# Kernel tuning notes

Measured on AMD Instinct MI355X. Metric: run time of the kernel, lower is better.

Reference implementation:

```python
import jax, jax.numpy as jnp
import numpy as np

N_CLI, N_AGG, E, D, L = 100000, 1000, 1600000, 128, 3


def setup_inputs() -> dict:
    key = jax.random.key(0)
    ks = jax.random.split(key, 16)
    inp = {
        'x_clients': jax.random.normal(ks[0], (N_CLI, D), jnp.float32),
        'x_agg': jax.random.normal(ks[1], (N_AGG, D), jnp.float32),
        'c2a_src': jax.random.randint(ks[2], (E,), 0, N_CLI, jnp.int32),
        'c2a_dst': jax.random.randint(ks[3], (E,), 0, N_AGG, jnp.int32),
        'a2c_src': jax.random.randint(ks[4], (E,), 0, N_AGG, jnp.int32),
        'a2c_dst': jax.random.randint(ks[5], (E,), 0, N_CLI, jnp.int32),
    }
    s = 1.0 / np.sqrt(D)
    # stacked per-layer SAGE params for each edge type: W_l (on aggregated msg), W_r (on dst), b
    inp['Wl_c2a'] = jax.random.uniform(ks[6], (L, D, D), jnp.float32, -s, s)
    inp['Wr_c2a'] = jax.random.uniform(ks[7], (L, D, D), jnp.float32, -s, s)
    inp['b_c2a'] = jax.random.uniform(ks[8], (L, D), jnp.float32, -s, s)
    inp['Wl_a2c'] = jax.random.uniform(ks[9], (L, D, D), jnp.float32, -s, s)
    inp['Wr_a2c'] = jax.random.uniform(ks[10], (L, D, D), jnp.float32, -s, s)
    inp['b_a2c'] = jax.random.uniform(ks[11], (L, D), jnp.float32, -s, s)
    inp['W_lin'] = jax.random.uniform(ks[12], (D, 1), jnp.float32, -s, s)
    inp['b_lin'] = jax.random.uniform(ks[13], (1,), jnp.float32, -s, s)
    return inp


def _sage(x_src, x_dst, src, dst, Wl, Wr, b, n_dst):
    # mean aggregation of gathered source features onto dst nodes
    msg = x_src[src]                                        # [E, D]
    summed = jax.ops.segment_sum(msg, dst, num_segments=n_dst)
    cnt = jax.ops.segment_sum(jnp.ones((src.shape[0], 1), x_src.dtype), dst, num_segments=n_dst)
    mean = summed / jnp.maximum(cnt, 1.0)
    return mean @ Wl + x_dst @ Wr + b


def _leaky(x):
    return jnp.where(x >= 0, x, 0.1 * x)


def reference(x_clients, x_agg, c2a_src, c2a_dst, a2c_src, a2c_dst,
              Wl_c2a, Wr_c2a, b_c2a, Wl_a2c, Wr_a2c, b_a2c, W_lin, b_lin):
    xc, xa = x_clients, x_agg
    for l in range(L):
        new_a = _sage(xc, xa, c2a_src, c2a_dst, Wl_c2a[l], Wr_c2a[l], b_c2a[l], N_AGG)
        new_c = _sage(xa, xc, a2c_src, a2c_dst, Wl_a2c[l], Wr_a2c[l], b_a2c[l], N_CLI)
        xa, xc = _leaky(new_a), _leaky(new_c)
    return (xc @ W_lin + b_lin).squeeze(1)
```

## Files before the change

### kernel.cpp

```cpp
#include <hip/hip_runtime.h>

#define D      128
#define NCLI   100000
#define NAGG   1000
#define NLAYER 3
#define NBKT   98
#define NC2A   63
#define NRNG   8
#define NBIN   (NAGG * NRNG)
#define RMAGIC 343598u
#define NHIST  512
#define NCVTX  (NCLI * D / 4 / 256)
#define NCVTW  ((NLAYER * D * D + 255) / 256)
#define NROWT  (NCLI / 32)
#define CPB    391

typedef short bf16x8 __attribute__((ext_vector_type(8)));
typedef float f32x16 __attribute__((ext_vector_type(16)));

static __device__ __forceinline__ float leaky(float x) { return x >= 0.f ? x : 0.1f * x; }

static __device__ __forceinline__ unsigned bf16_rn(float f) {
    unsigned u = __float_as_uint(f);
    return (u + 0x7fffu + ((u >> 16) & 1u)) >> 16;
}
static __device__ __forceinline__ float bf_val(unsigned h) { return __uint_as_float(h << 16); }
static __device__ __forceinline__ unsigned pack_bf2(float lo, float hi) {
    return bf16_rn(lo) | (bf16_rn(hi) << 16);
}
static __device__ __forceinline__ float bf_lo(unsigned v) { return __uint_as_float(v << 16); }
static __device__ __forceinline__ float bf_hi(unsigned v) { return __uint_as_float(v & 0xffff0000u); }

__global__ __launch_bounds__(256) void prep(const int* __restrict__ c2a_src,
                                            const int* __restrict__ c2a_dst,
                                            const int* __restrict__ a2c_dst, int E,
                                            int* __restrict__ cnt_ar, int* __restrict__ bcnt,
                                            const float4* __restrict__ X4,
                                            uint2* __restrict__ xhi, uint2* __restrict__ xlo,
                                            const float* __restrict__ W,
                                            unsigned short* __restrict__ Wt) {
    __shared__ int h[NBIN + NBKT];
    int bid = blockIdx.x;
    if (bid < NHIST) {
        for (int i = threadIdx.x; i < NBIN + NBKT; i += 256) h[i] = 0;
        __syncthreads();
        int stride = NHIST * 256;
        for (int e = bid * 256 + threadIdx.x; e < E; e += stride) {
            int s = c2a_src[e];
            int bin = c2a_dst[e] * NRNG + (int)__umulhi((unsigned)s, RMAGIC);
            atomicAdd(&h[bin], 1);
            atomicAdd(&h[NBIN + (a2c_dst[e] >> 10)], 1);
        }
        __syncthreads();
        for (int i = threadIdx.x; i < NBIN; i += 256)
            if (h[i]) atomicAdd(&cnt_ar[i], h[i]);
        for (int i = threadIdx.x; i < NBKT; i += 256)
            if (h[NBIN + i]) atomicAdd(&bcnt[i], h[NBIN + i]);
    } else if (bid < NHIST + NCVTX) {
        int t = (bid - NHIST) * 256 + threadIdx.x;
        float4 f = X4[t];
        unsigned h0 = bf16_rn(f.x), h1 = bf16_rn(f.y), h2 = bf16_rn(f.z), h3 = bf16_rn(f.w);
        xhi[t] = make_uint2(h0 | (h1 << 16), h2 | (h3 << 16));
        xlo[t] = make_uint2(pack_bf2(f.x - bf_val(h0), f.y - bf_val(h1)),
                            pack_bf2(f.z - bf_val(h2), f.w - bf_val(h3)));
    } else {
        int idx = (bid - NHIST - NCVTX) * 256 + threadIdx.x;
        if (idx >= NLAYER * D * D) return;
        int layer = idx >> 14, rem = idx & (D * D - 1);
        int k = rem >> 7, n = rem & 127;
        float w = W[layer * D * D + k * D + n];
        unsigned hh = bf16_rn(w);
        unsigned short* base = Wt + layer * 2 * D * D;
        base[n * D + k] = (unsigned short)hh;
        base[D * D + n * D + k] = (unsigned short)bf16_rn(w - bf_val(hh));
    }
}

__global__ void scan_both(const int* __restrict__ cnt_ar, int* __restrict__ rp_ar,
                          const int* __restrict__ bcnt,
                          int* __restrict__ brp, int* __restrict__ bcur,
                          int* __restrict__ ccur) {
    __shared__ int sh[1024];
    int t = threadIdx.x;
    if (blockIdx.x == 0) {
        int v[8];
        int s = 0;
#pragma unroll
        for (int j = 0; j < 8; j++) {
            int idx = t * 8 + j;
            v[j] = (idx < NBIN) ? cnt_ar[idx] : 0;
            s += v[j];
        }
        sh[t] = s;
        __syncthreads();
        for (int off = 1; off < 1024; off <<= 1) {
            int x = (t >= off) ? sh[t - off] : 0;
            __syncthreads();
            sh[t] += x;
            __syncthreads();
        }
        int run = sh[t] - s;
#pragma unroll
        for (int j = 0; j < 8; j++) {
            int idx = t * 8 + j;
            if (idx < NBIN) rp_ar[idx] = run;
            run += v[j];
        }
        if (t == 1023) rp_ar[NBIN] = sh[1023];
        __syncthreads();
        if (t < NC2A) ccur[t] = rp_ar[t * 128];
    } else {
        int v = (t < NBKT) ? bcnt[t] : 0;
        sh[t] = v;
        __syncthreads();
        for (int off = 1; off < 1024; off <<= 1) {
            int x = (t >= off) ? sh[t - off] : 0;
            __syncthreads();
            sh[t] += x;
            __syncthreads();
        }
        if (t == 0) { brp[0] = 0; bcur[0] = 0; }
        if (t < NBKT) {
            brp[t + 1] = sh[t];
            if (t + 1 < NBKT) bcur[t + 1] = sh[t];
        }
    }
}

__global__ __launch_bounds__(1024) void scatter_coarse(const int* __restrict__ c2a_src,
                                                       const int* __restrict__ c2a_dst,
                                                       const int* __restrict__ a2c_src,
                                                       const int* __restrict__ a2c_dst, int E,
                                                       int* __restrict__ ccur,
                                                       int* __restrict__ tmp1,
                                                       int* __restrict__ bcur,
                                                       int* __restrict__ tmp2) {
    __shared__ int h[NBKT], base[NBKT];
    int tid = threadIdx.x;
    if (blockIdx.x < 256) {
        int chunk = (E + 255) / 256;
        int e0 = blockIdx.x * chunk;
        int e1 = min(E, e0 + chunk);
        for (int i = tid; i < NC2A; i += 1024) h[i] = 0;
        __syncthreads();
        for (int e = e0 + tid; e < e1; e += 1024) {
            int s = c2a_src[e];
            int bin = c2a_dst[e] * NRNG + (int)__umulhi((unsigned)s, RMAGIC);
            atomicAdd(&h[bin >> 7], 1);
        }
        __syncthreads();
        for (int i = tid; i < NC2A; i += 1024) {
            int c = h[i];
            base[i] = c ? atomicAdd(&ccur[i], c) : 0;
        }
        __syncthreads();
        for (int e = e0 + tid; e < e1; e += 1024) {
            int s = c2a_src[e];
            int bin = c2a_dst[e] * NRNG + (int)__umulhi((unsigned)s, RMAGIC);
            int pos = atomicAdd(&base[bin >> 7], 1);
            tmp1[pos] = (bin << 17) | s;
        }
    } else {
        int bid = blockIdx.x - 256;
        int chunk = (E + 255) / 256;
        int e0 = bid * chunk;
        int e1 = min(E, e0 + chunk);
        for (int i = tid; i < NBKT; i += 1024) h[i] = 0;
        __syncthreads();
        for (int e = e0 + tid; e < e1; e += 1024) atomicAdd(&h[a2c_dst[e] >> 10], 1);
        __syncthreads();
        for (int i = tid; i < NBKT; i += 1024) {
            int c = h[i];
            base[i] = c ? atomicAdd(&bcur[i], c) : 0;
        }
        __syncthreads();
        for (int e = e0 + tid; e < e1; e += 1024) {
            int d = a2c_dst[e];
            int pos = atomicAdd(&base[d >> 10], 1);
            tmp2[pos] = ((d & 1023) << 10) | a2c_src[e];
        }
    }
}

__global__ __launch_bounds__(1024) void refine(const int* __restrict__ rp_ar,
                                               const int* __restrict__ tmp1,
                                               int* __restrict__ col_c2a,
                                               const int* __restrict__ brp,
                                               const int* __restrict__ tmp2,
                                               int* __restrict__ rp_c,
                                               int* __restrict__ col_a2c) {
    int tid = threadIdx.x;
    if (blockIdx.x < NC2A) {
        __shared__ int lcur[128];
        int c = blockIdx.x;
        int b0 = c * 128;
        int nb = min(128, NBIN - b0);
        if (tid < nb) lcur[tid] = rp_ar[b0 + tid];
        int beg = rp_ar[b0];
        int end = rp_ar[min(b0 + 128, NBIN)];
        __syncthreads();
        for (int e = beg + tid; e < end; e += 1024) {
            int v = tmp1[e];
            int pos = atomicAdd(&lcur[(v >> 17) - b0], 1);
            col_c2a[pos] = v & 0x1FFFF;
        }
    } else {
        __shared__ int h2[1024], cur2[1024];
        int b = blockIdx.x - NC2A;
        int beg = brp[b], end = brp[b + 1];
        h2[tid] = 0;
        __syncthreads();
        for (int e = beg + tid; e < end; e += 1024) atomicAdd(&h2[tmp2[e] >> 10], 1);
        __syncthreads();
        cur2[tid] = h2[tid];
        __syncthreads();
        for (int off = 1; off < 1024; off <<= 1) {
            int x = (tid >= off) ? cur2[tid - off] : 0;
            __syncthreads();
            cur2[tid] += x;
            __syncthreads();
        }
        int start = beg + cur2[tid] - h2[tid];
        int c = b * 1024 + tid;
        if (c < NCLI) rp_c[c] = start;
        cur2[tid] = start;
        if (b == NBKT - 1 && tid == 0) rp_c[NCLI] = end;
        __syncthreads();
        for (int e = beg + tid; e < end; e += 1024) {
            int p = tmp2[e];
            int pos = atomicAdd(&cur2[p >> 10], 1);
            col_a2c[pos] = p & 1023;
        }
    }
}


__global__ __launch_bounds__(512) void gather_mean(const unsigned* __restrict__ tbl,
                                                   const int* __restrict__ rp_ar,
                                                   const int* __restrict__ col,
                                                   float* __restrict__ psum) {
    __shared__ float part[4][8][D];
    int quad = blockIdx.x >> 3, r = blockIdx.x & 7;
    int tid = threadIdx.x;
    int a = tid >> 7;
    int sub = (tid >> 4) & 7;
    int sl = tid & 15;
    const uint4* tbl4 = (const uint4*)tbl;
    int agg = quad * 4 + a;
    int bin = agg * NRNG + r;
    int beg = rp_ar[bin], end = rp_ar[bin + 1];
    float f0 = 0, f1 = 0, f2 = 0, f3 = 0, f4 = 0, f5 = 0, f6 = 0, f7 = 0;
    int e = beg + sub;
    for (; e + 8 < end; e += 16) {
        int s0 = col[e];
        int s1 = col[e + 8];
        uint4 v0 = tbl4[(s0 << 4) + sl];
        uint4 v1 = tbl4[(s1 << 4) + sl];
        f0 += bf_lo(v0.x); f1 += bf_hi(v0.x); f2 += bf_lo(v0.y); f3 += bf_hi(v0.y);
        f4 += bf_lo(v0.z); f5 += bf_hi(v0.z); f6 += bf_lo(v0.w); f7 += bf_hi(v0.w);
        f0 += bf_lo(v1.x); f1 += bf_hi(v1.x); f2 += bf_lo(v1.y); f3 += bf_hi(v1.y);
        f4 += bf_lo(v1.z); f5 += bf_hi(v1.z); f6 += bf_lo(v1.w); f7 += bf_hi(v1.w);
    }
    if (e < end) {
        int s0 = col[e];
        uint4 v0 = tbl4[(s0 << 4) + sl];
        f0 += bf_lo(v0.x); f1 += bf_hi(v0.x); f2 += bf_lo(v0.y); f3 += bf_hi(v0.y);
        f4 += bf_lo(v0.z); f5 += bf_hi(v0.z); f6 += bf_lo(v0.w); f7 += bf_hi(v0.w);
    }
    float* pr = &part[a][sub][sl * 8];
    pr[0] = f0; pr[1] = f1; pr[2] = f2; pr[3] = f3;
    pr[4] = f4; pr[5] = f5; pr[6] = f6; pr[7] = f7;
    __syncthreads();
    int c = tid & 127;
    float s = 0.f;
#pragma unroll
    for (int g = 0; g < 8; g++) s += part[a][g][c];
    psum[((size_t)agg * NRNG + r) * D + c] = s;
}

template <int LAST>
__global__ __launch_bounds__(128) void combine_agg(const float* __restrict__ psum,
                                                   const int* __restrict__ rp_ar,
                                                   const float* xa_old,
                                                   const float* __restrict__ Wl_a2c,
                                                   const float* __restrict__ Wl_c2a,
                                                   const float* __restrict__ Wr_c2a,
                                                   const float* __restrict__ b_c2a,
                                                   unsigned short* __restrict__ ya_bf,
                                                   float* xa_out) {
    __shared__ float mr[D], xr[D];
    int i = blockIdx.x, j = threadIdx.x;
    if (LAST) {
        xr[j] = xa_old[i * D + j];
        __syncthreads();
        float accy = 0.f;
#pragma unroll 4
        for (int k = 0; k < D; k++) accy += xr[k] * Wl_a2c[k * D + j];
        ya_bf[i * D + j] = (unsigned short)bf16_rn(accy);
        return;
    }
    const float* pr = psum + (size_t)i * NRNG * D + j;
    float s = 0.f;
#pragma unroll
    for (int r = 0; r < NRNG; r++) s += pr[r * D];
    int deg = rp_ar[i * NRNG + NRNG] - rp_ar[i * NRNG];
    mr[j] = s / fmaxf((float)deg, 1.f);
    xr[j] = xa_old[i * D + j];
    __syncthreads();
    float accy = 0.f, accn = b_c2a[j];
#pragma unroll 4
    for (int k = 0; k < D; k++) {
        accy += xr[k] * Wl_a2c[k * D + j];
        accn += mr[k] * Wl_c2a[k * D + j] + xr[k] * Wr_c2a[k * D + j];
    }
    ya_bf[i * D + j] = (unsigned short)bf16_rn(accy);
    xa_out[i * D + j] = leaky(accn);
}

__global__ __launch_bounds__(256) void gemm_y(const unsigned short* __restrict__ Ahi,
                                              const unsigned short* __restrict__ Alo,
                                              const unsigned short* __restrict__ Wt,
                                              const float* __restrict__ bias,
                                              float* __restrict__ Yb) {
    int tid = threadIdx.x;
    int wave = tid >> 6, lane = tid & 63;
    int cl = lane & 31, kh = lane >> 5;
    int n0 = wave * 32;
    int m0 = blockIdx.x * 32;
    float bv = bias[n0 + cl];
    f32x16 acc;
#pragma unroll
    for (int qq = 0; qq < 16; qq++) acc[qq] = bv;
    {
        const unsigned short* Wlo_ = Wt + D * D;
        const unsigned short* ar = Ahi + (size_t)(m0 + cl) * D + kh * 8;
        const unsigned short* al = Alo + (size_t)(m0 + cl) * D + kh * 8;
        const unsigned short* wh = Wt + (size_t)(n0 + cl) * D + kh * 8;
        const unsigned short* wl = Wlo_ + (size_t)(n0 + cl) * D + kh * 8;
#pragma unroll
        for (int kc = 0; kc < 8; kc++) {
            bf16x8 ahi = *(const bf16x8*)(ar + kc * 16);
            bf16x8 alo = *(const bf16x8*)(al + kc * 16);
            bf16x8 bh = *(const bf16x8*)(wh + kc * 16);
            bf16x8 bl = *(const bf16x8*)(wl + kc * 16);
            acc = __builtin_amdgcn_mfma_f32_32x32x16_bf16(ahi, bh, acc, 0, 0, 0);
            acc = __builtin_amdgcn_mfma_f32_32x32x16_bf16(alo, bh, acc, 0, 0, 0);
            acc = __builtin_amdgcn_mfma_f32_32x32x16_bf16(ahi, bl, acc, 0, 0, 0);
        }
    }
    float* yb = Yb + (size_t)m0 * D + n0 + cl;
#pragma unroll
    for (int reg = 0; reg < 16; reg++) {
        int row = (reg & 3) + 8 * (reg >> 2) + 4 * kh;
        yb[(size_t)row * D] = acc[reg];
    }
}

template <int LAST>
__global__ __launch_bounds__(1024) void agg_big(const unsigned short* __restrict__ ya,
                                                const int* __restrict__ rowptr,
                                                const int* __restrict__ col,
                                                const float* __restrict__ Yb,
                                                unsigned* __restrict__ xhi,
                                                unsigned* __restrict__ xlo,
                                                const float* __restrict__ Wlin,
                                                const float* __restrict__ blin,
                                                float* __restrict__ out) {
    __shared__ uint4 yast4[NAGG * 9];
    int tid = threadIdx.x;
    int wave = tid >> 6, lane = tid & 63;
    int g = lane >> 3, q = lane & 7;
    int m0 = blockIdx.x * CPB;
    const uint4* ya4g = (const uint4*)ya;
    float dacc[4] = {0.f, 0.f, 0.f, 0.f};
#pragma unroll
    for (int h = 0; h < 2; h++) {
        if (h) __syncthreads();
        for (int i = tid; i < NAGG * 8; i += 1024) {
            int row = i >> 3, qq = i & 7;
            yast4[row * 9 + qq] = ya4g[(row << 4) + (h << 3) + qq];
        }
        __syncthreads();
#pragma unroll
        for (int cc = 0; cc < 4; cc++) {
            int c_local = (wave * 8 + g) * 4 + cc;
            int gid = m0 + c_local;
            bool act = (c_local < CPB) && (gid < NCLI);
            int beg = 0, end = 0;
            if (act) { beg = rowptr[gid]; end = rowptr[gid + 1]; }
            float s0 = 0, s1 = 0, s2 = 0, s3 = 0, s4 = 0, s5 = 0, s6 = 0, s7 = 0;
            for (int ch = beg; ch < end; ch += 8) {
                int ec = col[min(ch + q, end - 1)];
                int lim = min(8, end - ch);
#pragma unroll
                for (int j = 0; j < 8; j++) {
                    if (j < lim) {
                        int r = __shfl(ec, j, 8);
                        uint4 v = yast4[r * 9 + q];
                        s0 += bf_lo(v.x); s1 += bf_hi(v.x);
                        s2 += bf_lo(v.y); s3 += bf_hi(v.y);
                        s4 += bf_lo(v.z); s5 += bf_hi(v.z);
                        s6 += bf_lo(v.w); s7 += bf_hi(v.w);
                    }
                }
            }
            if (act) {
                float inv = 1.f / fmaxf((float)(end - beg), 1.f);
                const float4* yb4 =
                    (const float4*)(Yb + (size_t)gid * D + h * 64 + q * 8);
                float4 y0 = yb4[0], y1 = yb4[1];
                float r0 = leaky(y0.x + s0 * inv);
                float r1 = leaky(y0.y + s1 * inv);
                float r2 = leaky(y0.z + s2 * inv);
                float r3 = leaky(y0.w + s3 * inv);
                float r4 = leaky(y1.x + s4 * inv);
                float r5 = leaky(y1.y + s5 * inv);
                float r6 = leaky(y1.z + s6 * inv);
                float r7 = leaky(y1.w + s7 * inv);
                if (LAST) {
                    float4 w0 = *(const float4*)&Wlin[h * 64 + q * 8];
                    float4 w1 = *(const float4*)&Wlin[h * 64 + q * 8 + 4];
                    dacc[cc] += r0 * w0.x + r1 * w0.y + r2 * w0.z + r3 * w0.w +
                                r4 * w1.x + r5 * w1.y + r6 * w1.z + r7 * w1.w;
                    if (h == 1) {
                        float v = dacc[cc];
#pragma unroll
                        for (int off = 4; off > 0; off >>= 1) v += __shfl_down(v, off, 8);
                        if (q == 0) out[gid] = v + blin[0];
                    }
                } else {
                    unsigned h0 = bf16_rn(r0), h1 = bf16_rn(r1);
                    unsigned h2 = bf16_rn(r2), h3 = bf16_rn(r3);
                    unsigned h4 = bf16_rn(r4), h5 = bf16_rn(r5);
                    unsigned h6 = bf16_rn(r6), h7 = bf16_rn(r7);
                    uint4 hi, lo;
                    hi.x = h0 | (h1 << 16); hi.y = h2 | (h3 << 16);
                    hi.z = h4 | (h5 << 16); hi.w = h6 | (h7 << 16);
                    lo.x = pack_bf2(r0 - bf_val(h0), r1 - bf_val(h1));
                    lo.y = pack_bf2(r2 - bf_val(h2), r3 - bf_val(h3));
                    lo.z = pack_bf2(r4 - bf_val(h4), r5 - bf_val(h5));
                    lo.w = pack_bf2(r6 - bf_val(h6), r7 - bf_val(h7));
                    ((uint4*)xhi)[(gid << 4) + (h << 3) + q] = hi;
                    ((uint4*)xlo)[(gid << 4) + (h << 3) + q] = lo;
                }
            }
        }
    }
}

extern "C" void kernel_launch(void* const* d_in, const int* in_sizes, int n_in,
                              void* d_out, int out_size, void* d_ws, size_t ws_size,
                              hipStream_t stream) {
    const float* x_clients = (const float*)d_in[0];
    const float* x_agg     = (const float*)d_in[1];
    const int*   c2a_src   = (const int*)d_in[2];
    const int*   c2a_dst   = (const int*)d_in[3];
    const int*   a2c_src   = (const int*)d_in[4];
    const int*   a2c_dst   = (const int*)d_in[5];
    const float* Wl_c2a    = (const float*)d_in[6];
    const float* Wr_c2a    = (const float*)d_in[7];
    const float* b_c2a     = (const float*)d_in[8];
    const float* Wl_a2c    = (const float*)d_in[9];
    const float* Wr_a2c    = (const float*)d_in[10];
    const float* b_a2c     = (const float*)d_in[11];
    const float* W_lin     = (const float*)d_in[12];
    const float* b_lin     = (const float*)d_in[13];
    float* out = (float*)d_out;
    const int E = in_sizes[2];

    char* p = (char*)d_ws;
    auto alloc = [&](size_t bytes) {
        char* r = p;
        p += (bytes + 255) & ~(size_t)255;
        return r;
    };
    float*    Yb    = (float*)alloc(sizeof(float) * NCLI * D);
    unsigned* xc_hi = (unsigned*)alloc(sizeof(unsigned) * NCLI * 64);
    unsigned* xc_lo = (unsigned*)alloc(sizeof(unsigned) * NCLI * 64);
    float*    xa    = (float*)alloc(sizeof(float) * NAGG * D);
    unsigned short* ya_bf = (unsigned short*)alloc(sizeof(unsigned short) * NAGG * D);
    unsigned short* Wt = (unsigned short*)alloc(sizeof(unsigned short) * NLAYER * 2 * D * D);
    float* psum  = (float*)alloc(sizeof(float) * NAGG * NRNG * D);
    int* cnt_ar = (int*)alloc(sizeof(int) * (NBIN + NBKT));
    int* bcnt  = cnt_ar + NBIN;
    int* rp_ar = (int*)alloc(sizeof(int) * (NBIN + 1));
    int* brp   = (int*)alloc(sizeof(int) * (NBKT + 1));
    int* bcur  = (int*)alloc(sizeof(int) * NBKT);
    int* ccur  = (int*)alloc(sizeof(int) * NC2A);
    int* rp_c  = (int*)alloc(sizeof(int) * (NCLI + 1));
    int* col_c2a = (int*)alloc(sizeof(int) * E);
    int* col_a2c = (int*)alloc(sizeof(int) * E);
    int* tmp1 = (int*)Yb;
    int* tmp2 = tmp1 + E;

    hipMemsetAsync(cnt_ar, 0, sizeof(int) * (NBIN + NBKT), stream);

    prep<<<NHIST + NCVTX + NCVTW, 256, 0, stream>>>(c2a_src, c2a_dst, a2c_dst, E, cnt_ar, bcnt,
                                                    (const float4*)x_clients,
                                                    (uint2*)xc_hi, (uint2*)xc_lo,
                                                    Wr_a2c, Wt);
    scan_both<<<2, 1024, 0, stream>>>(cnt_ar, rp_ar, bcnt, brp, bcur, ccur);
    scatter_coarse<<<512, 1024, 0, stream>>>(c2a_src, c2a_dst, a2c_src, a2c_dst, E,
                                             ccur, tmp1, bcur, tmp2);
    refine<<<NC2A + NBKT, 1024, 0, stream>>>(rp_ar, tmp1, col_c2a, brp, tmp2, rp_c, col_a2c);

    const float* xa_old = x_agg;
    for (int l = 0; l < NLAYER; l++) {
        if (l < NLAYER - 1) {
            gather_mean<<<(NAGG / 4) * NRNG, 512, 0, stream>>>(xc_hi, rp_ar, col_c2a, psum);
            combine_agg<0><<<NAGG, 128, 0, stream>>>(psum, rp_ar, xa_old,
                                                     Wl_a2c + l * D * D, Wl_c2a + l * D * D,
                                                     Wr_c2a + l * D * D, b_c2a + l * D,
                                                     ya_bf, xa);
            gemm_y<<<NROWT, 256, 0, stream>>>(
                (const unsigned short*)xc_hi, (const unsigned short*)xc_lo,
                Wt + l * 2 * D * D, b_a2c + l * D, Yb);
            agg_big<0><<<256, 1024, 0, stream>>>(ya_bf, rp_c, col_a2c, Yb,
                                                 xc_hi, xc_lo, nullptr, nullptr, nullptr);
        } else {
            combine_agg<1><<<NAGG, 128, 0, stream>>>(psum, rp_ar, xa_old,
                                                     Wl_a2c + l * D * D, Wl_c2a + l * D * D,
                                                     Wr_c2a + l * D * D, b_c2a + l * D,
                                                     ya_bf, xa);
            gemm_y<<<NROWT, 256, 0, stream>>>(
                (const unsigned short*)xc_hi, (const unsigned short*)xc_lo,
                Wt + l * 2 * D * D, b_a2c + l * D, Yb);
            agg_big<1><<<256, 1024, 0, stream>>>(ya_bf, rp_c, col_a2c, Yb,
                                                 nullptr, nullptr, W_lin, b_lin, out);
        }
        xa_old = xa;
    }
}
```

Baseline: 609.5 us.

## Fuse gather_mean and gemm_y into one heterogeneous per-layer launch

Merges the independent c2a gather-mean and the client GEMM (Yb = xc@Wr + b) into a single kernel whose blocks are partitioned by blockIdx: GEMM tiles (two 32-row tiles per 512-thread block), gather blocks, and in the last layer small blocks computing ya = xa@Wl_a2c. This lets the memory-bound gather overlap with the MFMA-bound GEMM and removes launches and serialization between them. In exchange, register and LDS footprint are set by the largest branch, which may lower occupancy for the GEMM part. Early-return of odd tail tiles happens before no barrier in the GEMM branch, so it stays safe.

```diff
diff --git a/kernel.cpp b/kernel.cpp
--- a/kernel.cpp
+++ b/kernel.cpp
@@ -13,6 +13,9 @@
 #define NCVTX  (NCLI * D / 4 / 256)
 #define NCVTW  ((NLAYER * D * D + 255) / 256)
 #define NROWT  (NCLI / 32)
+#define NGEMM  ((NROWT + 1) / 2)
+#define NGATH  ((NAGG / 4) * NRNG)
+#define NLAST  (NAGG / 4)
 #define CPB    391
 
 typedef short bf16x8 __attribute__((ext_vector_type(8)));
@@ -235,50 +238,6 @@
 }
 
 
-__global__ __launch_bounds__(512) void gather_mean(const unsigned* __restrict__ tbl,
-                                                   const int* __restrict__ rp_ar,
-                                                   const int* __restrict__ col,
-                                                   float* __restrict__ psum) {
-    __shared__ float part[4][8][D];
-    int quad = blockIdx.x >> 3, r = blockIdx.x & 7;
-    int tid = threadIdx.x;
-    int a = tid >> 7;
-    int sub = (tid >> 4) & 7;
-    int sl = tid & 15;
-    const uint4* tbl4 = (const uint4*)tbl;
-    int agg = quad * 4 + a;
-    int bin = agg * NRNG + r;
-    int beg = rp_ar[bin], end = rp_ar[bin + 1];
-    float f0 = 0, f1 = 0, f2 = 0, f3 = 0, f4 = 0, f5 = 0, f6 = 0, f7 = 0;
-    int e = beg + sub;
-    for (; e + 8 < end; e += 16) {
-        int s0 = col[e];
-        int s1 = col[e + 8];
-        uint4 v0 = tbl4[(s0 << 4) + sl];
-        uint4 v1 = tbl4[(s1 << 4) + sl];
-        f0 += bf_lo(v0.x); f1 += bf_hi(v0.x); f2 += bf_lo(v0.y); f3 += bf_hi(v0.y);
-        f4 += bf_lo(v0.z); f5 += bf_hi(v0.z); f6 += bf_lo(v0.w); f7 += bf_hi(v0.w);
-        f0 += bf_lo(v1.x); f1 += bf_hi(v1.x); f2 += bf_lo(v1.y); f3 += bf_hi(v1.y);
-        f4 += bf_lo(v1.z); f5 += bf_hi(v1.z); f6 += bf_lo(v1.w); f7 += bf_hi(v1.w);
-    }
-    if (e < end) {
-        int s0 = col[e];
-        uint4 v0 = tbl4[(s0 << 4) + sl];
-        f0 += bf_lo(v0.x); f1 += bf_hi(v0.x); f2 += bf_lo(v0.y); f3 += bf_hi(v0.y);
-        f4 += bf_lo(v0.z); f5 += bf_hi(v0.z); f6 += bf_lo(v0.w); f7 += bf_hi(v0.w);
-    }
-    float* pr = &part[a][sub][sl * 8];
-    pr[0] = f0; pr[1] = f1; pr[2] = f2; pr[3] = f3;
-    pr[4] = f4; pr[5] = f5; pr[6] = f6; pr[7] = f7;
-    __syncthreads();
-    int c = tid & 127;
-    float s = 0.f;
-#pragma unroll
-    for (int g = 0; g < 8; g++) s += part[a][g][c];
-    psum[((size_t)agg * NRNG + r) * D + c] = s;
-}
-
-template <int LAST>
 __global__ __launch_bounds__(128) void combine_agg(const float* __restrict__ psum,
                                                    const int* __restrict__ rp_ar,
                                                    const float* xa_old,
@@ -290,15 +249,6 @@
                                                    float* xa_out) {
     __shared__ float mr[D], xr[D];
     int i = blockIdx.x, j = threadIdx.x;
-    if (LAST) {
-        xr[j] = xa_old[i * D + j];
-        __syncthreads();
-        float accy = 0.f;
-#pragma unroll 4
-        for (int k = 0; k < D; k++) accy += xr[k] * Wl_a2c[k * D + j];
-        ya_bf[i * D + j] = (unsigned short)bf16_rn(accy);
-        return;
-    }
     const float* pr = psum + (size_t)i * NRNG * D + j;
     float s = 0.f;
 #pragma unroll
@@ -317,42 +267,100 @@
     xa_out[i * D + j] = leaky(accn);
 }
 
-__global__ __launch_bounds__(256) void gemm_y(const unsigned short* __restrict__ Ahi,
-                                              const unsigned short* __restrict__ Alo,
-                                              const unsigned short* __restrict__ Wt,
-                                              const float* __restrict__ bias,
-                                              float* __restrict__ Yb) {
-    int tid = threadIdx.x;
-    int wave = tid >> 6, lane = tid & 63;
-    int cl = lane & 31, kh = lane >> 5;
-    int n0 = wave * 32;
-    int m0 = blockIdx.x * 32;
-    float bv = bias[n0 + cl];
-    f32x16 acc;
-#pragma unroll
-    for (int qq = 0; qq < 16; qq++) acc[qq] = bv;
-    {
-        const unsigned short* Wlo_ = Wt + D * D;
-        const unsigned short* ar = Ahi + (size_t)(m0 + cl) * D + kh * 8;
-        const unsigned short* al = Alo + (size_t)(m0 + cl) * D + kh * 8;
-        const unsigned short* wh = Wt + (size_t)(n0 + cl) * D + kh * 8;
-        const unsigned short* wl = Wlo_ + (size_t)(n0 + cl) * D + kh * 8;
-#pragma unroll
-        for (int kc = 0; kc < 8; kc++) {
-            bf16x8 ahi = *(const bf16x8*)(ar + kc * 16);
-            bf16x8 alo = *(const bf16x8*)(al + kc * 16);
-            bf16x8 bh = *(const bf16x8*)(wh + kc * 16);
-            bf16x8 bl = *(const bf16x8*)(wl + kc * 16);
-            acc = __builtin_amdgcn_mfma_f32_32x32x16_bf16(ahi, bh, acc, 0, 0, 0);
-            acc = __builtin_amdgcn_mfma_f32_32x32x16_bf16(alo, bh, acc, 0, 0, 0);
-            acc = __builtin_amdgcn_mfma_f32_32x32x16_bf16(ahi, bl, acc, 0, 0, 0);
-        }
-    }
-    float* yb = Yb + (size_t)m0 * D + n0 + cl;
-#pragma unroll
-    for (int reg = 0; reg < 16; reg++) {
-        int row = (reg & 3) + 8 * (reg >> 2) + 4 * kh;
-        yb[(size_t)row * D] = acc[reg];
+__global__ __launch_bounds__(512) void layer_par(
+    const unsigned short* __restrict__ Ahi, const unsigned short* __restrict__ Alo,
+    const unsigned short* __restrict__ Wt, const float* __restrict__ bias,
+    float* __restrict__ Yb,
+    const unsigned* __restrict__ tbl, const int* __restrict__ rp_ar,
+    const int* __restrict__ col, float* __restrict__ psum, int ngath,
+    const float* __restrict__ xa_old, const float* __restrict__ Wl_a2c,
+    unsigned short* __restrict__ ya_bf) {
+    __shared__ float part[4][8][D];
+    int bid = blockIdx.x;
+    if (bid < NGEMM) {
+        int tile = bid * 2 + (threadIdx.x >> 8);
+        if (tile >= NROWT) return;
+        int tid = threadIdx.x & 255;
+        int wave = tid >> 6, lane = tid & 63;
+        int cl = lane & 31, kh = lane >> 5;
+        int n0 = wave * 32;
+        int m0 = tile * 32;
+        float bv = bias[n0 + cl];
+        f32x16 acc;
+#pragma unroll
+        for (int qq = 0; qq < 16; qq++) acc[qq] = bv;
+        {
+            const unsigned short* Wlo_ = Wt + D * D;
+            const unsigned short* ar = Ahi + (size_t)(m0 + cl) * D + kh * 8;
+            const unsigned short* al = Alo + (size_t)(m0 + cl) * D + kh * 8;
+            const unsigned short* wh = Wt + (size_t)(n0 + cl) * D + kh * 8;
+            const unsigned short* wl = Wlo_ + (size_t)(n0 + cl) * D + kh * 8;
+#pragma unroll
+            for (int kc = 0; kc < 8; kc++) {
+                bf16x8 ahi = *(const bf16x8*)(ar + kc * 16);
+                bf16x8 alo = *(const bf16x8*)(al + kc * 16);
+                bf16x8 bh = *(const bf16x8*)(wh + kc * 16);
+                bf16x8 bl = *(const bf16x8*)(wl + kc * 16);
+                acc = __builtin_amdgcn_mfma_f32_32x32x16_bf16(ahi, bh, acc, 0, 0, 0);
+                acc = __builtin_amdgcn_mfma_f32_32x32x16_bf16(alo, bh, acc, 0, 0, 0);
+                acc = __builtin_amdgcn_mfma_f32_32x32x16_bf16(ahi, bl, acc, 0, 0, 0);
+            }
+        }
+        float* yb = Yb + (size_t)m0 * D + n0 + cl;
+#pragma unroll
+        for (int reg = 0; reg < 16; reg++) {
+            int row = (reg & 3) + 8 * (reg >> 2) + 4 * kh;
+            yb[(size_t)row * D] = acc[reg];
+        }
+    } else if (bid < NGEMM + ngath) {
+        int g = bid - NGEMM;
+        int quad = g >> 3, r = g & 7;
+        int tid = threadIdx.x;
+        int a = tid >> 7;
+        int sub = (tid >> 4) & 7;
+        int sl = tid & 15;
+        const uint4* tbl4 = (const uint4*)tbl;
+        int agg = quad * 4 + a;
+        int bin = agg * NRNG + r;
+        int beg = rp_ar[bin], end = rp_ar[bin + 1];
+        float f0 = 0, f1 = 0, f2 = 0, f3 = 0, f4 = 0, f5 = 0, f6 = 0, f7 = 0;
+        int e = beg + sub;
+        for (; e + 8 < end; e += 16) {
+            int s0 = col[e];
+            int s1 = col[e + 8];
+            uint4 v0 = tbl4[(s0 << 4) + sl];
+            uint4 v1 = tbl4[(s1 << 4) + sl];
+            f0 += bf_lo(v0.x); f1 += bf_hi(v0.x); f2 += bf_lo(v0.y); f3 += bf_hi(v0.y);
+            f4 += bf_lo(v0.z); f5 += bf_hi(v0.z); f6 += bf_lo(v0.w); f7 += bf_hi(v0.w);
+            f0 += bf_lo(v1.x); f1 += bf_hi(v1.x); f2 += bf_lo(v1.y); f3 += bf_hi(v1.y);
+            f4 += bf_lo(v1.z); f5 += bf_hi(v1.z); f6 += bf_lo(v1.w); f7 += bf_hi(v1.w);
+        }
+        if (e < end) {
+            int s0 = col[e];
+            uint4 v0 = tbl4[(s0 << 4) + sl];
+            f0 += bf_lo(v0.x); f1 += bf_hi(v0.x); f2 += bf_lo(v0.y); f3 += bf_hi(v0.y);
+            f4 += bf_lo(v0.z); f5 += bf_hi(v0.z); f6 += bf_lo(v0.w); f7 += bf_hi(v0.w);
+        }
+        float* pr = &part[a][sub][sl * 8];
+        pr[0] = f0; pr[1] = f1; pr[2] = f2; pr[3] = f3;
+        pr[4] = f4; pr[5] = f5; pr[6] = f6; pr[7] = f7;
+        __syncthreads();
+        int c = tid & 127;
+        float s = 0.f;
+#pragma unroll
+        for (int gg = 0; gg < 8; gg++) s += part[a][gg][c];
+        psum[((size_t)agg * NRNG + r) * D + c] = s;
+    } else {
+        int grp = threadIdx.x >> 7;
+        int ab = (bid - NGEMM - ngath) * 4 + grp;
+        int j = threadIdx.x & 127;
+        float* xr = &part[0][0][0] + grp * D;
+        xr[j] = xa_old[ab * D + j];
+        __syncthreads();
+        float accy = 0.f;
+#pragma unroll 4
+        for (int k = 0; k < D; k++) accy += xr[k] * Wl_a2c[k * D + j];
+        ya_bf[ab * D + j] = (unsigned short)bf16_rn(accy);
     }
 }
 
@@ -507,24 +515,23 @@
     const float* xa_old = x_agg;
     for (int l = 0; l < NLAYER; l++) {
         if (l < NLAYER - 1) {
-            gather_mean<<<(NAGG / 4) * NRNG, 512, 0, stream>>>(xc_hi, rp_ar, col_c2a, psum);
-            combine_agg<0><<<NAGG, 128, 0, stream>>>(psum, rp_ar, xa_old,
-                                                     Wl_a2c + l * D * D, Wl_c2a + l * D * D,
-                                                     Wr_c2a + l * D * D, b_c2a + l * D,
-                                                     ya_bf, xa);
-            gemm_y<<<NROWT, 256, 0, stream>>>(
+            layer_par<<<NGEMM + NGATH, 512, 0, stream>>>(
                 (const unsigned short*)xc_hi, (const unsigned short*)xc_lo,
-                Wt + l * 2 * D * D, b_a2c + l * D, Yb);
+                Wt + l * 2 * D * D, b_a2c + l * D, Yb,
+                xc_hi, rp_ar, col_c2a, psum, NGATH,
+                xa_old, Wl_a2c + l * D * D, ya_bf);
+            combine_agg<<<NAGG, 128, 0, stream>>>(psum, rp_ar, xa_old,
+                                                  Wl_a2c + l * D * D, Wl_c2a + l * D * D,
+                                                  Wr_c2a + l * D * D, b_c2a + l * D,
+                                                  ya_bf, xa);
             agg_big<0><<<256, 1024, 0, stream>>>(ya_bf, rp_c, col_a2c, Yb,
                                                  xc_hi, xc_lo, nullptr, nullptr, nullptr);
         } else {
-            combine_agg<1><<<NAGG, 128, 0, stream>>>(psum, rp_ar, xa_old,
-                                                     Wl_a2c + l * D * D, Wl_c2a + l * D * D,
-                                                     Wr_c2a + l * D * D, b_c2a + l * D,
-                                                     ya_bf, xa);
-            gemm_y<<<NROWT, 256, 0, stream>>>(
+            layer_par<<<NGEMM + NLAST, 512, 0, stream>>>(
                 (const unsigned short*)xc_hi, (const unsigned short*)xc_lo,
-                Wt + l * 2 * D * D, b_a2c + l * D, Yb);
+                Wt + l * 2 * D * D, b_a2c + l * D, Yb,
+                xc_hi, rp_ar, col_c2a, psum, 0,
+                xa_old, Wl_a2c + l * D * D, ya_bf);
             agg_big<1><<<256, 1024, 0, stream>>>(ya_bf, rp_c, col_a2c, Yb,
                                                  nullptr, nullptr, W_lin, b_lin, out);
         }
```

New measurement: 604.6 us. About the same (-0.8%).
